# Performance work log

Hardware: AMD Instinct MI355X
Metric: run time of the kernel (lower is better)

## Reference

```python
import jax, jax.numpy as jnp
import numpy as np

B, L, H = 8, 2048, 2048
N_ACTIONS = 8
NEG_INF = -1e30


def setup_inputs() -> dict:
    key = jax.random.key(0)
    k1, k2, k3, k4, k5 = jax.random.split(key, 5)
    stdv = 1.0 / np.sqrt(H)
    return {
        "x": jax.random.normal(k1, (B, L, H), dtype=jnp.float32),
        "y": jax.random.normal(k2, (B, H), dtype=jnp.float32),
        "x_mask": jnp.zeros((B, L), dtype=bool),
        "actions": jax.random.randint(k3, (B,), 0, N_ACTIONS),
        "weight": jax.random.uniform(k4, (H, H), jnp.float32, -stdv, stdv),  # [y_size, x_size]
        "bias": jnp.zeros((H,), dtype=jnp.float32),
        "wa": jax.random.uniform(k5, (N_ACTIONS, H, H), jnp.float32, -stdv, stdv),
        "ba": jnp.zeros((N_ACTIONS, H), dtype=jnp.float32),
    }


def reference(x, y, x_mask, actions, weight, bias, wa, ba):
    # Gather the per-sample action weights (math-identical to the original
    # compute-all-then-one-hot-select loop, without the O(n_actions) waste).
    wa_sel = wa[actions]                      # [B, h2, h1]
    ba_sel = ba[actions]                      # [B, h1]
    # func='mul_s': W_a = weight * sigmoid(wa[a]); b_a = bias * sigmoid(ba[a])
    W = weight[None, :, :] * jax.nn.sigmoid(wa_sel)   # [B, h2, h1]
    Wy = jnp.einsum('bh,bhx->bx', y, W) + bias[None, :] * jax.nn.sigmoid(ba_sel)  # [B, h1]
    xWy = jnp.einsum('blh,bh->bl', x, Wy)     # [B, L]
    xWy = jnp.where(x_mask, NEG_INF, xWy)
    # eval-mode path of the original (softmax); training uses log_softmax
    return jax.nn.softmax(xWy, axis=-1)
```

## Files before the change

### kernel.cpp

```cpp
#include <hip/hip_runtime.h>
#include <hip/hip_bf16.h>
#include <math.h>

#define B 8
#define L 2048
#define H 2048
#define NA 8
#define NEG_INF (-1e30f)

#define XT 64
#define COLS 32

__device__ __forceinline__ float sigf(float t) {
    return 1.0f / (1.0f + __expf(-t));
}

__global__ __launch_bounds__(256) void k_wy(
    const float* __restrict__ y, const int* __restrict__ actions,
    const float* __restrict__ weight, const float* __restrict__ wa,
    const float* __restrict__ bias, const float* __restrict__ ba,
    float* __restrict__ Wy)
{
    const int b  = blockIdx.y;
    const int x0 = blockIdx.x * COLS;
    const int a  = actions[b];
    const int c4 = threadIdx.x & 7;
    const int hg = threadIdx.x >> 3;

    __shared__ float ylds[H];
    for (int i = threadIdx.x * 4; i < H; i += 1024)
        *(float4*)(ylds + i) = *(const float4*)(y + (size_t)b * H + i);
    __syncthreads();

    const float* __restrict__ wp = weight + x0 + c4 * 4;
    const float* __restrict__ ap = wa + (size_t)a * H * H + x0 + c4 * 4;

    float4 acc = make_float4(0.f, 0.f, 0.f, 0.f);
    #pragma unroll 8
    for (int h = hg; h < H; h += 32) {
        const float  yv = ylds[h];
        const float4 w4 = *(const float4*)(wp + (size_t)h * H);
        const float4 a4 = *(const float4*)(ap + (size_t)h * H);
        acc.x += yv * w4.x * sigf(a4.x);
        acc.y += yv * w4.y * sigf(a4.y);
        acc.z += yv * w4.z * sigf(a4.z);
        acc.w += yv * w4.w * sigf(a4.w);
    }

    __shared__ float4 red[32][8];
    red[hg][c4] = acc;
    __syncthreads();
    #pragma unroll
    for (int s = 16; s; s >>= 1) {
        if (hg < s) {
            const float4 v = red[hg + s][c4];
            acc.x += v.x; acc.y += v.y; acc.z += v.z; acc.w += v.w;
            red[hg][c4] = acc;
        }
        __syncthreads();
    }

    if (hg == 0) {
        const float4 bi  = *(const float4*)(bias + x0 + c4 * 4);
        const float4 bav = *(const float4*)(ba + (size_t)a * H + x0 + c4 * 4);
        acc.x += bi.x * sigf(bav.x);
        acc.y += bi.y * sigf(bav.y);
        acc.z += bi.z * sigf(bav.z);
        acc.w += bi.w * sigf(bav.w);
        *(float4*)(Wy + (size_t)b * H + x0 + c4 * 4) = acc;
    }
}

__global__ __launch_bounds__(256) void k_xwy(
    const float* __restrict__ x, const float* __restrict__ Wy,
    const unsigned char* __restrict__ mask, float* __restrict__ xWy)
{
    const int wave = threadIdx.x >> 6;
    const int lane = threadIdx.x & 63;
    const int row  = blockIdx.x * 4 + wave;
    const int b    = (blockIdx.x * 4) >> 11;

    __shared__ float wlds[H];
    for (int i = threadIdx.x * 4; i < H; i += 1024)
        *(float4*)(wlds + i) = *(const float4*)(Wy + (size_t)b * H + i);
    __syncthreads();

    const float* __restrict__ xb = x + (size_t)row * H;

    float acc = 0.f;
    #pragma unroll
    for (int j = 0; j < H / 256; ++j) {
        const int off = j * 256 + lane * 4;
        const float4 xv = *(const float4*)(xb + off);
        const float4 wv = *(const float4*)(wlds + off);
        acc += xv.x * wv.x + xv.y * wv.y + xv.z * wv.z + xv.w * wv.w;
    }
    #pragma unroll
    for (int s = 32; s; s >>= 1) acc += __shfl_xor(acc, s, 64);
    if (lane == 0) xWy[row] = mask[row] ? NEG_INF : acc;
}

__global__ __launch_bounds__(256) void k_softmax(
    const float* __restrict__ xWy, float* __restrict__ out)
{
    const int b    = blockIdx.x;
    const int tid  = threadIdx.x;
    const int wave = tid >> 6;
    const int lane = tid & 63;
    const float* __restrict__ v = xWy + (size_t)b * L;

    float vals[L / 256];
    float m = -INFINITY;
    #pragma unroll
    for (int j = 0; j < L / 256; ++j) {
        vals[j] = v[tid + j * 256];
        m = fmaxf(m, vals[j]);
    }
    #pragma unroll
    for (int s = 32; s; s >>= 1) m = fmaxf(m, __shfl_xor(m, s, 64));

    __shared__ float redm[4];
    if (lane == 0) redm[wave] = m;
    __syncthreads();
    m = fmaxf(fmaxf(redm[0], redm[1]), fmaxf(redm[2], redm[3]));

    float sum = 0.f;
    #pragma unroll
    for (int j = 0; j < L / 256; ++j) {
        vals[j] = __expf(vals[j] - m);
        sum += vals[j];
    }
    #pragma unroll
    for (int s = 32; s; s >>= 1) sum += __shfl_xor(sum, s, 64);

    __shared__ float reds[4];
    if (lane == 0) reds[wave] = sum;
    __syncthreads();
    sum = reds[0] + reds[1] + reds[2] + reds[3];

    const float inv = 1.0f / sum;
    #pragma unroll
    for (int j = 0; j < L / 256; ++j)
        out[(size_t)b * L + tid + j * 256] = vals[j] * inv;
}

extern "C" void kernel_launch(void* const* d_in, const int* in_sizes, int n_in,
                              void* d_out, int out_size, void* d_ws, size_t ws_size,
                              hipStream_t stream) {
    const float*         x       = (const float*)d_in[0];
    const float*         y       = (const float*)d_in[1];
    const unsigned char* mask    = (const unsigned char*)d_in[2];
    const int*           actions = (const int*)d_in[3];
    const float*         weight  = (const float*)d_in[4];
    const float*         bias    = (const float*)d_in[5];
    const float*         wa      = (const float*)d_in[6];
    const float*         ba      = (const float*)d_in[7];
    float*               out     = (float*)d_out;

    float* ws  = (float*)d_ws;
    float* Wy  = ws;
    float* xWy = Wy + (size_t)B * H;

    dim3 g1(XT, B);
    k_wy<<<g1, 256, 0, stream>>>(y, actions, weight, wa, bias, ba, Wy);
    k_xwy<<<B * L / 4, 256, 0, stream>>>(x, Wy, mask, xWy);
    k_softmax<<<B, 256, 0, stream>>>(xWy, out);
}
```

Baseline: 54.90 us.

## Group batches by shared action and split-K the Wy reduction

Result: slower. 70.25 us (+28.0%).

```diff
diff --git a/kernel.cpp b/kernel.cpp
--- a/kernel.cpp
+++ b/kernel.cpp
@@ -19,85 +19,147 @@
     const float* __restrict__ y, const int* __restrict__ actions,
     const float* __restrict__ weight, const float* __restrict__ wa,
     const float* __restrict__ bias, const float* __restrict__ ba,
-    float* __restrict__ Wy)
+    float* __restrict__ Wyp)
 {
-    const int b  = blockIdx.y;
-    const int x0 = blockIdx.x * COLS;
-    const int a  = actions[b];
+    const int xt = blockIdx.x;
+    const int s  = blockIdx.y;
+    const int x0 = xt * COLS;
     const int c4 = threadIdx.x & 7;
     const int hg = threadIdx.x >> 3;
 
-    __shared__ float ylds[H];
-    for (int i = threadIdx.x * 4; i < H; i += 1024)
-        *(float4*)(ylds + i) = *(const float4*)(y + (size_t)b * H + i);
-    __syncthreads();
-
-    const float* __restrict__ wp = weight + x0 + c4 * 4;
-    const float* __restrict__ ap = wa + (size_t)a * H * H + x0 + c4 * 4;
-
-    float4 acc = make_float4(0.f, 0.f, 0.f, 0.f);
-    #pragma unroll 8
-    for (int h = hg; h < H; h += 32) {
-        const float  yv = ylds[h];
-        const float4 w4 = *(const float4*)(wp + (size_t)h * H);
-        const float4 a4 = *(const float4*)(ap + (size_t)h * H);
-        acc.x += yv * w4.x * sigf(a4.x);
-        acc.y += yv * w4.y * sigf(a4.y);
-        acc.z += yv * w4.z * sigf(a4.z);
-        acc.w += yv * w4.w * sigf(a4.w);
-    }
-
-    __shared__ float4 red[32][8];
-    red[hg][c4] = acc;
-    __syncthreads();
-    #pragma unroll
-    for (int s = 16; s; s >>= 1) {
-        if (hg < s) {
-            const float4 v = red[hg + s][c4];
-            acc.x += v.x; acc.y += v.y; acc.z += v.z; acc.w += v.w;
-            red[hg][c4] = acc;
+    __shared__ float ylds[B * H];
+    __shared__ int s_ga[8], s_gmask[8], s_ng;
+
+    if (threadIdx.x == 0) {
+        int acts[8];
+        for (int b2 = 0; b2 < 8; ++b2) acts[b2] = actions[b2];
+        int ng = 0;
+        for (int b2 = 0; b2 < 8; ++b2) {
+            bool isnew = true;
+            for (int p = 0; p < b2; ++p) if (acts[p] == acts[b2]) isnew = false;
+            if (isnew) {
+                int m = 0;
+                for (int q = 0; q < 8; ++q) if (acts[q] == acts[b2]) m |= 1 << q;
+                s_ga[ng] = acts[b2]; s_gmask[ng] = m; ++ng;
+            }
+        }
+        s_ng = ng;
+    }
+    for (int i = threadIdx.x * 4; i < B * H; i += 1024)
+        *(float4*)(ylds + i) = *(const float4*)(y + i);
+    __syncthreads();
+
+    const int ng     = s_ng;
+    const int fStart = s * ng * (H / 8);
+    const int fEnd   = fStart + ng * (H / 8);
+
+    float4 acc[8];
+    #pragma unroll
+    for (int b2 = 0; b2 < 8; ++b2) acc[b2] = make_float4(0.f, 0.f, 0.f, 0.f);
+
+    for (int g = fStart / H; g * H < fEnd; ++g) {
+        const int h0   = max(fStart - g * H, 0);
+        const int h1   = min(fEnd - g * H, H);
+        const int mask = __builtin_amdgcn_readfirstlane(s_gmask[g]);
+        const int a    = __builtin_amdgcn_readfirstlane(s_ga[g]);
+        const float* __restrict__ wp = weight + x0 + c4 * 4;
+        const float* __restrict__ ap = wa + (size_t)a * H * H + x0 + c4 * 4;
+        #pragma unroll 4
+        for (int h = h0 + hg; h < h1; h += 32) {
+            const float4 w4 = *(const float4*)(wp + (size_t)h * H);
+            const float4 a4 = *(const float4*)(ap + (size_t)h * H);
+            float4 s4;
+            s4.x = w4.x * sigf(a4.x);
+            s4.y = w4.y * sigf(a4.y);
+            s4.z = w4.z * sigf(a4.z);
+            s4.w = w4.w * sigf(a4.w);
+            #pragma unroll
+            for (int b2 = 0; b2 < 8; ++b2) {
+                if (mask & (1 << b2)) {
+                    const float yv = ylds[b2 * H + h];
+                    acc[b2].x += yv * s4.x;
+                    acc[b2].y += yv * s4.y;
+                    acc[b2].z += yv * s4.z;
+                    acc[b2].w += yv * s4.w;
+                }
+            }
+        }
+    }
+
+    __syncthreads();
+    float4* red = (float4*)ylds;
+    #pragma unroll
+    for (int b2 = 0; b2 < 8; ++b2) red[(b2 * 32 + hg) * 8 + c4] = acc[b2];
+    __syncthreads();
+    #pragma unroll
+    for (int st = 16; st; st >>= 1) {
+        if (hg < st) {
+            #pragma unroll
+            for (int b2 = 0; b2 < 8; ++b2) {
+                float4 o = red[(b2 * 32 + hg + st) * 8 + c4];
+                float4 m2 = red[(b2 * 32 + hg) * 8 + c4];
+                m2.x += o.x; m2.y += o.y; m2.z += o.z; m2.w += o.w;
+                red[(b2 * 32 + hg) * 8 + c4] = m2;
+            }
         }
         __syncthreads();
     }
 
     if (hg == 0) {
-        const float4 bi  = *(const float4*)(bias + x0 + c4 * 4);
-        const float4 bav = *(const float4*)(ba + (size_t)a * H + x0 + c4 * 4);
-        acc.x += bi.x * sigf(bav.x);
-        acc.y += bi.y * sigf(bav.y);
-        acc.z += bi.z * sigf(bav.z);
-        acc.w += bi.w * sigf(bav.w);
-        *(float4*)(Wy + (size_t)b * H + x0 + c4 * 4) = acc;
+        #pragma unroll
+        for (int b2 = 0; b2 < 8; ++b2) {
+            float4 v = red[(b2 * 32) * 8 + c4];
+            if (s == 0) {
+                const int ab = actions[b2];
+                const float4 bi  = *(const float4*)(bias + x0 + c4 * 4);
+                const float4 bav = *(const float4*)(ba + (size_t)ab * H + x0 + c4 * 4);
+                v.x += bi.x * sigf(bav.x);
+                v.y += bi.y * sigf(bav.y);
+                v.z += bi.z * sigf(bav.z);
+                v.w += bi.w * sigf(bav.w);
+            }
+            *(float4*)(Wyp + ((size_t)(b2 * 8 + s)) * H + x0 + c4 * 4) = v;
+        }
     }
 }
 
 __global__ __launch_bounds__(256) void k_xwy(
-    const float* __restrict__ x, const float* __restrict__ Wy,
+    const float* __restrict__ x, const float* __restrict__ Wyp,
     const unsigned char* __restrict__ mask, float* __restrict__ xWy)
 {
     const int wave = threadIdx.x >> 6;
     const int lane = threadIdx.x & 63;
-    const int row  = blockIdx.x * 4 + wave;
-    const int b    = (blockIdx.x * 4) >> 11;
+    const int row0 = blockIdx.x * 8;
+    const int b    = row0 >> 11;
 
     __shared__ float wlds[H];
-    for (int i = threadIdx.x * 4; i < H; i += 1024)
-        *(float4*)(wlds + i) = *(const float4*)(Wy + (size_t)b * H + i);
-    __syncthreads();
-
-    const float* __restrict__ xb = x + (size_t)row * H;
-
-    float acc = 0.f;
-    #pragma unroll
-    for (int j = 0; j < H / 256; ++j) {
-        const int off = j * 256 + lane * 4;
-        const float4 xv = *(const float4*)(xb + off);
-        const float4 wv = *(const float4*)(wlds + off);
-        acc += xv.x * wv.x + xv.y * wv.y + xv.z * wv.z + xv.w * wv.w;
-    }
-    #pragma unroll
-    for (int s = 32; s; s >>= 1) acc += __shfl_xor(acc, s, 64);
-    if (lane == 0) xWy[row] = mask[row] ? NEG_INF : acc;
+    for (int i = threadIdx.x * 4; i < H; i += 1024) {
+        float4 sum = make_float4(0.f, 0.f, 0.f, 0.f);
+        #pragma unroll
+        for (int s = 0; s < 8; ++s) {
+            const float4 v = *(const float4*)(Wyp + ((size_t)(b * 8 + s)) * H + i);
+            sum.x += v.x; sum.y += v.y; sum.z += v.z; sum.w += v.w;
+        }
+        *(float4*)(wlds + i) = sum;
+    }
+    __syncthreads();
+
+    #pragma unroll
+    for (int r = 0; r < 2; ++r) {
+        const int row = row0 + wave * 2 + r;
+        const float* __restrict__ xb = x + (size_t)row * H;
+        float acc = 0.f;
+        #pragma unroll
+        for (int j = 0; j < H / 256; ++j) {
+            const int off = j * 256 + lane * 4;
+            const float4 xv = *(const float4*)(xb + off);
+            const float4 wv = *(const float4*)(wlds + off);
+            acc += xv.x * wv.x + xv.y * wv.y + xv.z * wv.z + xv.w * wv.w;
+        }
+        #pragma unroll
+        for (int sh = 32; sh; sh >>= 1) acc += __shfl_xor(acc, sh, 64);
+        if (lane == 0) xWy[row] = mask[row] ? NEG_INF : acc;
+    }
 }
 
 __global__ __launch_bounds__(256) void k_softmax(
@@ -158,11 +220,11 @@
     float*               out     = (float*)d_out;
 
     float* ws  = (float*)d_ws;
-    float* Wy  = ws;
-    float* xWy = Wy + (size_t)B * H;
-
-    dim3 g1(XT, B);
-    k_wy<<<g1, 256, 0, stream>>>(y, actions, weight, wa, bias, ba, Wy);
-    k_xwy<<<B * L / 4, 256, 0, stream>>>(x, Wy, mask, xWy);
+    float* Wyp = ws;
+    float* xWy = Wyp + (size_t)B * 8 * H;
+
+    dim3 g1(XT, 8);
+    k_wy<<<g1, 256, 0, stream>>>(y, actions, weight, wa, bias, ba, Wyp);
+    k_xwy<<<B * L / 8, 256, 0, stream>>>(x, Wyp, mask, xWy);
     k_softmax<<<B, 256, 0, stream>>>(xWy, out);
 }
```
